# Kernel tuning notes

Measured on AMD Instinct MI355X. Metric: run time of the kernel, lower is better.

The kernel has to match this reference:

```python
import jax, jax.numpy as jnp
import numpy as np

EPS = 1e-12  # torch F.normalize eps

def _l2norm(x):
    n = jnp.sqrt(jnp.sum(x * x, axis=-1, keepdims=True))
    return x / jnp.maximum(n, EPS)

def setup_inputs() -> dict:
    key = jax.random.key(0)
    k1, k2 = jax.random.split(key)
    B, C, H, W = 4, 256, 48, 48
    qkv = jax.random.normal(k1, (B, 3 * C, H, W), dtype=jnp.float32)
    temp = jnp.ones((8, 1, 1), dtype=jnp.float32)
    proj_w = jax.random.normal(k2, (C, C), dtype=jnp.float32) * (1.0 / np.sqrt(C))
    proj_b = jnp.zeros((C,), dtype=jnp.float32)
    return {"qkv": qkv, "temp": temp, "proj_w": proj_w, "proj_b": proj_b, "h": H, "w": W}

def reference(qkv, temp, proj_w, proj_b, h, w):
    num_heads = temp.shape[0]
    b = qkv.shape[0]
    q, k, v = jnp.split(qkv, 3, axis=1)

    def to_heads(x):
        # b (head c) h w -> b head (h w) c
        return x.reshape(b, num_heads, -1, h * w).transpose(0, 1, 3, 2)

    q = _l2norm(to_heads(q))
    k = _l2norm(to_heads(k))
    v = to_heads(v)

    # [b, head, N, N], temp (head,1,1) broadcasts over (n, m)
    attn = jnp.einsum('bhnc,bhmc->bhnm', q, k) * temp
    attn = jax.nn.softmax(jax.nn.relu(attn), axis=-1)
    out = jnp.einsum('bhnm,bhmc->bhnc', attn, v)
    # b head N c -> b head c N -> b (head c) h w
    out = out.transpose(0, 1, 3, 2).reshape(b, -1, h, w)
    # 1x1 conv == channel matmul
    out = jnp.einsum('oc,bchw->bohw', proj_w, out) + proj_b[None, :, None, None]
    return out
```

## Files before the change

### kernel.cpp

```cpp
#include <hip/hip_runtime.h>

typedef unsigned short u16;
typedef unsigned int   u32;
typedef __attribute__((ext_vector_type(8))) short short8;
typedef __attribute__((ext_vector_type(4))) float f32x4;

#define NB    4
#define NCH   256
#define NHD   8
#define HD    32
#define NSP   2304
#define NBH   32
#define NKT   36
#define KPW   9

__device__ __forceinline__ u16 f2bf(float f) {
    u32 u = __float_as_uint(f);
    u += 0x7FFFu + ((u >> 16) & 1u);
    return (u16)(u >> 16);
}
__device__ __forceinline__ u32 pack2(float a, float b) {
    return (u32)f2bf(a) | ((u32)f2bf(b) << 16);
}
__device__ __forceinline__ u32 pkfast(float a, float b) {
#if __has_builtin(__builtin_amdgcn_cvt_pk_bf16_f32)
    typedef __attribute__((ext_vector_type(2))) __bf16 bf2;
    union { bf2 v; u32 u; } cv;
    cv.v = __builtin_amdgcn_cvt_pk_bf16_f32(a, b);
    return cv.u;
#else
    return __builtin_amdgcn_perm(__float_as_uint(b), __float_as_uint(a), 0x07060302u);
#endif
}
__device__ __forceinline__ float fexp2(float x) {
#if __has_builtin(__builtin_amdgcn_exp2f)
    return __builtin_amdgcn_exp2f(x);
#else
    return exp2f(x);
#endif
}

__global__ __launch_bounds__(256) void prep_kernel(
    const float* __restrict__ qkv, const float* __restrict__ temp,
    const float* __restrict__ projw,
    u16* __restrict__ Qn, u16* __restrict__ Kn, u16* __restrict__ Vp,
    u16* __restrict__ Wb)
{
    const int p  = blockIdx.y;
    const int bh = blockIdx.z, b = bh >> 3, head = bh & 7;

    if (p == 3) {
        const int idx = (bh * (NSP / 256) + blockIdx.x) * 256 + threadIdx.x;
        if (idx < NCH * NCH / 4) {
            float4 v = ((const float4*)projw)[idx];
            ((uint2*)Wb)[idx] = make_uint2(pack2(v.x, v.y), pack2(v.z, v.w));
        }
        return;
    }

    const int n = blockIdx.x * 256 + threadIdx.x;
    const float* src = qkv + ((size_t)(b * 3 * NCH + p * NCH + head * HD)) * NSP + n;

    float v[HD];
#pragma unroll
    for (int d = 0; d < HD; ++d) v[d] = src[(size_t)d * NSP];

    if (p == 2) {
        const int tile = n >> 6, loc = n & 63;
        const int c = loc >> 5, r5 = loc & 31;
        const int qd  = (r5 < 16) ? (r5 >> 2) : ((r5 - 16) >> 2);
        const int jj  = (r5 < 16) ? (r5 & 3) : (4 + (r5 & 3));
        u16* dst = Vp + (size_t)bh * NSP * HD + (size_t)tile * 2048 + c * 32 + qd * 8 + jj;
#pragma unroll
        for (int d = 0; d < HD; ++d) dst[d * 64] = f2bf(v[d]);
    } else {
        float s = 0.f;
#pragma unroll
        for (int d = 0; d < HD; ++d) s += v[d] * v[d];
        float sc = 1.f / fmaxf(sqrtf(s), 1e-12f);
        if (p == 0) sc *= temp[head] * 1.44269504088896f;
        u32 pk[HD / 2];
#pragma unroll
        for (int i = 0; i < HD / 2; ++i) pk[i] = pack2(v[2 * i] * sc, v[2 * i + 1] * sc);
        u16* dst = (p == 0 ? Qn : Kn) + ((size_t)bh * NSP + n) * HD;
#pragma unroll
        for (int i = 0; i < 4; ++i) ((uint4*)dst)[i] = ((const uint4*)pk)[i];
    }
}

__global__ __launch_bounds__(256) void attn_kernel(
    const u16* __restrict__ Qn, const u16* __restrict__ Kn,
    const u16* __restrict__ Vp, u16* __restrict__ X)
{
    __shared__ float cmb[4][64][49];
    const int bh = blockIdx.x, b = bh >> 3, head = bh & 7;
    const int w = threadIdx.x >> 6, lane = threadIdx.x & 63;
    const int l15 = lane & 15, quad = lane >> 4;
    const int qbase = blockIdx.y * 64;

    const u16* Kg = Kn + (size_t)bh * NSP * HD + (size_t)w * KPW * 2048 + l15 * HD + quad * 8;
    const u16* Vg = Vp + (size_t)bh * NSP * HD + (size_t)w * KPW * 2048 + l15 * 64 + quad * 8;

    short8 qf[4];
#pragma unroll
    for (int t2 = 0; t2 < 4; ++t2)
        qf[t2] = *(const short8*)(Qn + ((size_t)bh * NSP + qbase + t2 * 16 + l15) * HD + quad * 8);

    const short one = (short)0x3F80;
    const short8 vones = {one, one, one, one, one, one, one, one};

    f32x4 oacc[4][2] = {{{0,0,0,0},{0,0,0,0}},{{0,0,0,0},{0,0,0,0}},
                        {{0,0,0,0},{0,0,0,0}},{{0,0,0,0},{0,0,0,0}}};
    f32x4 rsac[4]    = {{0,0,0,0},{0,0,0,0},{0,0,0,0},{0,0,0,0}};

    short8 ka[4];
#pragma unroll
    for (int i = 0; i < 4; ++i) ka[i] = *(const short8*)(Kg + i * 512);

    for (int kt = 0; kt < KPW; ++kt) {
        short8 vb[2][2];
#pragma unroll
        for (int c = 0; c < 2; ++c)
#pragma unroll
            for (int h = 0; h < 2; ++h)
                vb[c][h] = *(const short8*)(Vg + (size_t)kt * 2048 + h * 1024 + c * 32);
        short8 kan[4];
        if (kt + 1 < KPW) {
            const u16* Kp2 = Kg + (size_t)(kt + 1) * 2048;
#pragma unroll
            for (int i = 0; i < 4; ++i) kan[i] = *(const short8*)(Kp2 + i * 512);
        }

#pragma unroll
        for (int t2 = 0; t2 < 4; ++t2) {
            f32x4 sf[4];
#pragma unroll
            for (int i = 0; i < 4; ++i)
                sf[i] = __builtin_amdgcn_mfma_f32_16x16x32_bf16(ka[i], qf[t2], (f32x4){0.f,0.f,0.f,0.f}, 0, 0, 0);
            u32 pk[4][2];
#pragma unroll
            for (int i = 0; i < 4; ++i) {
                pk[i][0] = pkfast(fexp2(fmaxf(sf[i][0], 0.f)), fexp2(fmaxf(sf[i][1], 0.f)));
                pk[i][1] = pkfast(fexp2(fmaxf(sf[i][2], 0.f)), fexp2(fmaxf(sf[i][3], 0.f)));
            }
#pragma unroll
            for (int c = 0; c < 2; ++c) {
                union { short8 s; u32 u[4]; } pa;
                pa.u[0] = pk[2 * c][0];     pa.u[1] = pk[2 * c][1];
                pa.u[2] = pk[2 * c + 1][0]; pa.u[3] = pk[2 * c + 1][1];
                oacc[t2][0] = __builtin_amdgcn_mfma_f32_16x16x32_bf16(pa.s, vb[c][0], oacc[t2][0], 0, 0, 0);
                oacc[t2][1] = __builtin_amdgcn_mfma_f32_16x16x32_bf16(pa.s, vb[c][1], oacc[t2][1], 0, 0, 0);
                rsac[t2]    = __builtin_amdgcn_mfma_f32_16x16x32_bf16(pa.s, vones,    rsac[t2],    0, 0, 0);
            }
        }

        if (kt + 1 < KPW) {
#pragma unroll
            for (int i = 0; i < 4; ++i) ka[i] = kan[i];
        }
    }

    {
        float* my = &cmb[w][lane][0];
#pragma unroll
        for (int t2 = 0; t2 < 4; ++t2) {
#pragma unroll
            for (int h = 0; h < 2; ++h)
#pragma unroll
                for (int r = 0; r < 4; ++r) my[t2 * 12 + h * 4 + r] = oacc[t2][h][r];
#pragma unroll
            for (int r = 0; r < 4; ++r) my[t2 * 12 + 8 + r] = rsac[t2][r];
        }
    }
    __syncthreads();
    {
        const int t2 = w;
        float o0[4] = {0,0,0,0}, o1[4] = {0,0,0,0}, rsum[4] = {0,0,0,0};
#pragma unroll
        for (int j = 0; j < 4; ++j) {
            const float* srcp = &cmb[j][lane][t2 * 12];
#pragma unroll
            for (int r = 0; r < 4; ++r) {
                o0[r]   += srcp[r];
                o1[r]   += srcp[4 + r];
                rsum[r] += srcp[8 + r];
            }
        }
        u16* Xb = X + (size_t)b * NSP * NCH + head * HD;
#pragma unroll
        for (int r = 0; r < 4; ++r) {
            const float inv = 1.f / rsum[r];
            u16* row = Xb + (size_t)(qbase + t2 * 16 + quad * 4 + r) * NCH;
            row[l15]      = f2bf(o0[r] * inv);
            row[16 + l15] = f2bf(o1[r] * inv);
        }
    }
}

__global__ __launch_bounds__(64) void proj_kernel(
    const u16* __restrict__ Wb, const u16* __restrict__ X,
    const float* __restrict__ bias, float* __restrict__ out)
{
    const int b = blockIdx.z;
    const int lane = threadIdx.x;
    const int l15 = lane & 15, quad = lane >> 4;
    const int obase = blockIdx.y * 16;
    const int nbase = blockIdx.x * 32;

    const u16* wrow = Wb + (size_t)(obase + l15) * NCH + quad * 8;
    const u16* xrow = X + ((size_t)b * NSP + nbase + l15) * NCH + quad * 8;

    f32x4 acc[2] = {{0,0,0,0},{0,0,0,0}};
#pragma unroll
    for (int ks = 0; ks < 8; ++ks) {
        const short8 af = *(const short8*)(wrow + ks * 32);
        acc[0] = __builtin_amdgcn_mfma_f32_16x16x32_bf16(af, *(const short8*)(xrow + ks * 32), acc[0], 0, 0, 0);
        acc[1] = __builtin_amdgcn_mfma_f32_16x16x32_bf16(af, *(const short8*)(xrow + (size_t)16 * NCH + ks * 32), acc[1], 0, 0, 0);
    }
#pragma unroll
    for (int r = 0; r < 4; ++r) {
        const int o = obase + quad * 4 + r;
        const float bo = bias[o];
        float* orow = out + ((size_t)b * NCH + o) * NSP + nbase;
        orow[l15]      = acc[0][r] + bo;
        orow[16 + l15] = acc[1][r] + bo;
    }
}

extern "C" void kernel_launch(void* const* d_in, const int* in_sizes, int n_in,
                              void* d_out, int out_size, void* d_ws, size_t ws_size,
                              hipStream_t stream) {
    const float* qkv   = (const float*)d_in[0];
    const float* temp  = (const float*)d_in[1];
    const float* projw = (const float*)d_in[2];
    const float* projb = (const float*)d_in[3];
    float* out = (float*)d_out;

    u16* Qn = (u16*)d_ws;
    u16* Kn = Qn + (size_t)NBH * NSP * HD;
    u16* Vp = Kn + (size_t)NBH * NSP * HD;
    u16* X  = Vp + (size_t)NBH * NSP * HD;
    u16* Wb = X + (size_t)NB * NSP * NCH;

    prep_kernel<<<dim3(NSP / 256, 4, NBH), dim3(256), 0, stream>>>(qkv, temp, projw, Qn, Kn, Vp, Wb);
    attn_kernel<<<dim3(NBH, NSP / 64), dim3(256), 0, stream>>>(Qn, Kn, Vp, X);
    proj_kernel<<<dim3(NSP / 32, NCH / 16, NB), dim3(64), 0, stream>>>(Wb, X, projb, out);
}
```

Measured before the change: 147.8 us.

## Coalesce V scatter via LDS, trim attn combine, enlarge proj tiles

The V-prep path now stages its bf16 permuted layout in shared memory and writes it out as coalesced 16-byte stores, replacing scattered 2-byte global writes. In the attention epilogue each wave keeps its own tile's partials in registers and stores only the other three to shared memory, which shrinks the LDS buffer. The kt loop is unrolled by 3. The projection kernel moves to 256-thread blocks covering 64x64 output tiles, giving more weight reuse per load and fewer blocks, at the cost of extra shared memory in prep and more registers in proj.

```diff
diff --git a/kernel.cpp b/kernel.cpp
--- a/kernel.cpp
+++ b/kernel.cpp
@@ -66,13 +66,22 @@
     for (int d = 0; d < HD; ++d) v[d] = src[(size_t)d * NSP];
 
     if (p == 2) {
-        const int tile = n >> 6, loc = n & 63;
-        const int c = loc >> 5, r5 = loc & 31;
-        const int qd  = (r5 < 16) ? (r5 >> 2) : ((r5 - 16) >> 2);
-        const int jj  = (r5 < 16) ? (r5 & 3) : (4 + (r5 & 3));
-        u16* dst = Vp + (size_t)bh * NSP * HD + (size_t)tile * 2048 + c * 32 + qd * 8 + jj;
-#pragma unroll
-        for (int d = 0; d < HD; ++d) dst[d * 64] = f2bf(v[d]);
+        __shared__ u16 Lt[4][32][72];
+        const int tile = threadIdx.x >> 6;
+        const int r6 = threadIdx.x & 63;
+        const int c = r6 >> 5, r5 = r6 & 31;
+        const int qd = (r5 < 16) ? (r5 >> 2) : ((r5 - 16) >> 2);
+        const int jj = (r5 < 16) ? (r5 & 3) : (4 + (r5 & 3));
+        const int pos = c * 32 + qd * 8 + jj;
+#pragma unroll
+        for (int d = 0; d < HD; ++d) Lt[tile][d][pos] = f2bf(v[d]);
+        __syncthreads();
+        const int dd = r6 >> 1, half = r6 & 1;
+        const uint4* lsrc = (const uint4*)&Lt[tile][dd][half * 32];
+        const int gt = blockIdx.x * 4 + tile;
+        uint4* dst = (uint4*)(Vp + (size_t)bh * NSP * HD + (size_t)gt * 2048 + dd * 64 + half * 32);
+#pragma unroll
+        for (int i = 0; i < 4; ++i) dst[i] = lsrc[i];
     } else {
         float s = 0.f;
 #pragma unroll
@@ -92,7 +101,7 @@
     const u16* __restrict__ Qn, const u16* __restrict__ Kn,
     const u16* __restrict__ Vp, u16* __restrict__ X)
 {
-    __shared__ float cmb[4][64][49];
+    __shared__ float cmb[4][64][37];
     const int bh = blockIdx.x, b = bh >> 3, head = bh & 7;
     const int w = threadIdx.x >> 6, lane = threadIdx.x & 63;
     const int l15 = lane & 15, quad = lane >> 4;
@@ -117,6 +126,7 @@
 #pragma unroll
     for (int i = 0; i < 4; ++i) ka[i] = *(const short8*)(Kg + i * 512);
 
+#pragma unroll 3
     for (int kt = 0; kt < KPW; ++kt) {
         short8 vb[2][2];
 #pragma unroll
@@ -163,22 +173,29 @@
     {
         float* my = &cmb[w][lane][0];
 #pragma unroll
-        for (int t2 = 0; t2 < 4; ++t2) {
+        for (int s = 0; s < 3; ++s) {
+            const int t2 = s + (s >= w ? 1 : 0);
 #pragma unroll
             for (int h = 0; h < 2; ++h)
 #pragma unroll
-                for (int r = 0; r < 4; ++r) my[t2 * 12 + h * 4 + r] = oacc[t2][h][r];
-#pragma unroll
-            for (int r = 0; r < 4; ++r) my[t2 * 12 + 8 + r] = rsac[t2][r];
+                for (int r = 0; r < 4; ++r) my[s * 12 + h * 4 + r] = oacc[t2][h][r];
+#pragma unroll
+            for (int r = 0; r < 4; ++r) my[s * 12 + 8 + r] = rsac[t2][r];
         }
     }
     __syncthreads();
     {
         const int t2 = w;
-        float o0[4] = {0,0,0,0}, o1[4] = {0,0,0,0}, rsum[4] = {0,0,0,0};
+        float o0[4], o1[4], rsum[4];
+#pragma unroll
+        for (int r = 0; r < 4; ++r) {
+            o0[r] = oacc[t2][0][r]; o1[r] = oacc[t2][1][r]; rsum[r] = rsac[t2][r];
+        }
 #pragma unroll
         for (int j = 0; j < 4; ++j) {
-            const float* srcp = &cmb[j][lane][t2 * 12];
+            if (j == w) continue;
+            const int slot = w - (w > j ? 1 : 0);
+            const float* srcp = &cmb[j][lane][slot * 12];
 #pragma unroll
             for (int r = 0; r < 4; ++r) {
                 o0[r]   += srcp[r];
@@ -197,33 +214,37 @@
     }
 }
 
-__global__ __launch_bounds__(64) void proj_kernel(
+__global__ __launch_bounds__(256) void proj_kernel(
     const u16* __restrict__ Wb, const u16* __restrict__ X,
     const float* __restrict__ bias, float* __restrict__ out)
 {
     const int b = blockIdx.z;
-    const int lane = threadIdx.x;
+    const int w = threadIdx.x >> 6, lane = threadIdx.x & 63;
     const int l15 = lane & 15, quad = lane >> 4;
-    const int obase = blockIdx.y * 16;
-    const int nbase = blockIdx.x * 32;
+    const int obase = blockIdx.y * 64 + w * 16;
+    const int nbase = blockIdx.x * 64;
 
     const u16* wrow = Wb + (size_t)(obase + l15) * NCH + quad * 8;
     const u16* xrow = X + ((size_t)b * NSP + nbase + l15) * NCH + quad * 8;
 
-    f32x4 acc[2] = {{0,0,0,0},{0,0,0,0}};
+    f32x4 acc[4] = {{0,0,0,0},{0,0,0,0},{0,0,0,0},{0,0,0,0}};
 #pragma unroll
     for (int ks = 0; ks < 8; ++ks) {
         const short8 af = *(const short8*)(wrow + ks * 32);
-        acc[0] = __builtin_amdgcn_mfma_f32_16x16x32_bf16(af, *(const short8*)(xrow + ks * 32), acc[0], 0, 0, 0);
-        acc[1] = __builtin_amdgcn_mfma_f32_16x16x32_bf16(af, *(const short8*)(xrow + (size_t)16 * NCH + ks * 32), acc[1], 0, 0, 0);
+#pragma unroll
+        for (int jn = 0; jn < 4; ++jn) {
+            const short8 bf = *(const short8*)(xrow + (size_t)jn * 16 * NCH + ks * 32);
+            acc[jn] = __builtin_amdgcn_mfma_f32_16x16x32_bf16(af, bf, acc[jn], 0, 0, 0);
+        }
     }
 #pragma unroll
     for (int r = 0; r < 4; ++r) {
         const int o = obase + quad * 4 + r;
         const float bo = bias[o];
         float* orow = out + ((size_t)b * NCH + o) * NSP + nbase;
-        orow[l15]      = acc[0][r] + bo;
-        orow[16 + l15] = acc[1][r] + bo;
+#pragma unroll
+        for (int jn = 0; jn < 4; ++jn)
+            orow[jn * 16 + l15] = acc[jn][r] + bo;
     }
 }
 
@@ -244,5 +265,5 @@
 
     prep_kernel<<<dim3(NSP / 256, 4, NBH), dim3(256), 0, stream>>>(qkv, temp, projw, Qn, Kn, Vp, Wb);
     attn_kernel<<<dim3(NBH, NSP / 64), dim3(256), 0, stream>>>(Qn, Kn, Vp, X);
-    proj_kernel<<<dim3(NSP / 32, NCH / 16, NB), dim3(64), 0, stream>>>(Wb, X, projb, out);
-}
+    proj_kernel<<<dim3(NSP / 64, NCH / 64, NB), dim3(256), 0, stream>>>(Wb, X, projb, out);
+}
```

Result: slower. 153.1 us (+3.6%).
